# Kernel optimization log

Hardware: AMD Instinct MI355X
Metric: run time of the kernel (lower is better)

## Reference

```python
import jax, jax.numpy as jnp
import numpy as np

B, IN, OUT, N, K = 2048, 4096, 4096, 64, 4  # batch, in_features, out_features, num_nodes, degree


def setup_inputs() -> dict:
    key = jax.random.key(0)
    k0, k1, k2, k3 = jax.random.split(key, 4)
    x = jax.random.normal(k0, (B, IN), dtype=jnp.float32)
    # kaiming-ish init for the linear weight
    W = jax.random.normal(k1, (OUT, IN), dtype=jnp.float32) * (1.0 / np.sqrt(IN))
    ecoeff = jax.random.uniform(k2, (N, N), dtype=jnp.float32, minval=0.1, maxval=0.5)
    phase = jax.random.uniform(k3, (N, N), dtype=jnp.float32, minval=0.0, maxval=2.0 * np.pi)
    tension = jnp.ones((N,), dtype=jnp.float32)
    # deterministic degree-K ring topology: paths[i] = [(i+1..i+K) % N]
    src = jnp.repeat(jnp.arange(N), K).astype(jnp.int32)            # [E]
    dst = ((src + jnp.tile(jnp.arange(1, K + 1), N)) % N).astype(jnp.int32)  # [E]
    return {"x": x, "W": W, "ecoeff": ecoeff, "phase": phase,
            "tension": tension, "src": src, "dst": dst}


def reference(x, W, ecoeff, phase, tension, src, dst):
    # EntangledConnectionLayer.forward
    b = x.shape[0]
    out_features = W.shape[0]
    n = tension.shape[0]
    opn = out_features // n  # out_per_node

    out = x @ W.T  # [B, OUT] == F.linear(x, weights)
    nodes = out.reshape(b, n, opn)  # [B, N, opn] node-sliced view of output

    # entangled_connection_function on a real signal:
    # real(sig * (1 + eps*exp(i*phi)) / (1 + tau_i*tau_j)) = sig*(1+eps*cos(phi))/(1+tau_i*tau_j)
    eps = ecoeff[src, dst]                    # [E]
    phi = phase[src, dst]                     # [E]
    tau = tension[src] * tension[dst]         # [E]
    scale = (1.0 + eps * jnp.cos(phi)) / (1.0 + tau)  # [E]

    contrib = nodes[:, src, :] * scale[None, :, None]  # [B, E, opn]
    entangled = jnp.zeros_like(nodes).at[:, dst, :].add(contrib)  # scatter-add over edges

    return out + 0.5 * entangled.reshape(b, out_features)
```

## Files before the change

kernel.cpp:

```cpp
#include <hip/hip_runtime.h>
#include <hip/hip_bf16.h>

#define TILE 128
#define BK 64

typedef __attribute__((ext_vector_type(8))) short bf16x8;
typedef __attribute__((ext_vector_type(4))) float f32x4;

__device__ __forceinline__ unsigned short f32_to_bf16(float f) {
    unsigned u = __float_as_uint(f);
    unsigned rounded = u + 0x7FFF + ((u >> 16) & 1);
    return (unsigned short)(rounded >> 16);
}
__device__ __forceinline__ float bf16_to_f32(unsigned short h) {
    return __uint_as_float(((unsigned)h) << 16);
}
__device__ __forceinline__ bool probe_f32(const void* tens) {
    return ((const unsigned short*)tens)[0] == 0;
}

__global__ __launch_bounds__(256)
void prep_kernel(const void* __restrict__ xv, const void* __restrict__ Wv,
                 const void* __restrict__ ecoeff, const void* __restrict__ phase,
                 const void* __restrict__ tens,
                 const int* __restrict__ srcIdx, const int* __restrict__ dstIdx,
                 unsigned short* __restrict__ xa, unsigned short* __restrict__ wp,
                 int E, int K, int castB)
{
    constexpr int NODES = 64, CHUNK = 256, CAP = 8;
    __shared__ float buf[NODES * CHUNK];
    __shared__ int   cnt[NODES];
    __shared__ int   slist[NODES * CAP];
    __shared__ float clist[NODES * CAP];

    const bool isF32 = probe_f32(tens);
    const int tid = threadIdx.x;
    const int b   = blockIdx.x;

    if (b < castB) {
        const size_t i = ((size_t)b * 256 + tid) * 8;
        if (isF32) {
            const float4 a = *(const float4*)((const float*)xv + i);
            const float4 c = *(const float4*)((const float*)xv + i + 4);
            unsigned short p[8];
            p[0]=f32_to_bf16(a.x); p[1]=f32_to_bf16(a.y); p[2]=f32_to_bf16(a.z); p[3]=f32_to_bf16(a.w);
            p[4]=f32_to_bf16(c.x); p[5]=f32_to_bf16(c.y); p[6]=f32_to_bf16(c.z); p[7]=f32_to_bf16(c.w);
            *(bf16x8*)(xa + i) = *(const bf16x8*)p;
        } else {
            *(bf16x8*)(xa + i) = *(const bf16x8*)((const unsigned short*)xv + i);
        }
        return;
    }

    const int wb = b - castB;
    const int j  = wb & 63;
    const int k0 = (wb >> 6) * CHUNK;

    if (tid < NODES) cnt[tid] = 0;
    __syncthreads();
    if (tid < E) {
        const int s = srcIdx[tid];
        const int d = dstIdx[tid];
        float eps, phi, ts, td;
        if (isF32) {
            eps = ((const float*)ecoeff)[s * NODES + d];
            phi = ((const float*)phase)[s * NODES + d];
            ts  = ((const float*)tens)[s];
            td  = ((const float*)tens)[d];
        } else {
            eps = bf16_to_f32(((const unsigned short*)ecoeff)[s * NODES + d]);
            phi = bf16_to_f32(((const unsigned short*)phase)[s * NODES + d]);
            ts  = bf16_to_f32(((const unsigned short*)tens)[s]);
            td  = bf16_to_f32(((const unsigned short*)tens)[d]);
        }
        const float coef = 0.5f * (1.0f + eps * __cosf(phi)) / (1.0f + ts * td);
        const int pos = atomicAdd(&cnt[d], 1);
        if (pos < CAP) { slist[d * CAP + pos] = s; clist[d * CAP + pos] = coef; }
    }

    if (isF32) {
        for (int idx = tid; idx < NODES * CHUNK / 4; idx += 256) {
            const int s = idx >> 6;
            const int p = idx & 63;
            *(float4*)&buf[s * CHUNK + p * 4] = *(const float4*)
                ((const float*)Wv + (size_t)(s * 64 + j) * K + k0 + p * 4);
        }
    } else {
        for (int idx = tid; idx < NODES * CHUNK / 4; idx += 256) {
            const int s = idx >> 6;
            const int p = idx & 63;
            const ushort4 v = *(const ushort4*)
                ((const unsigned short*)Wv + (size_t)(s * 64 + j) * K + k0 + p * 4);
            buf[s * CHUNK + p * 4 + 0] = bf16_to_f32(v.x);
            buf[s * CHUNK + p * 4 + 1] = bf16_to_f32(v.y);
            buf[s * CHUNK + p * 4 + 2] = bf16_to_f32(v.z);
            buf[s * CHUNK + p * 4 + 3] = bf16_to_f32(v.w);
        }
    }
    __syncthreads();

    const int kk4  = (tid & 63) * 4;
    const int dgrp = (tid >> 6) * 16;
#pragma unroll 4
    for (int dd = 0; dd < 16; ++dd) {
        const int d = dgrp + dd;
        float v0 = buf[d * CHUNK + kk4 + 0];
        float v1 = buf[d * CHUNK + kk4 + 1];
        float v2 = buf[d * CHUNK + kk4 + 2];
        float v3 = buf[d * CHUNK + kk4 + 3];
        const int n = cnt[d] < CAP ? cnt[d] : CAP;
        for (int t = 0; t < n; ++t) {
            const float c = clist[d * CAP + t];
            const int   s = slist[d * CAP + t];
            v0 += c * buf[s * CHUNK + kk4 + 0];
            v1 += c * buf[s * CHUNK + kk4 + 1];
            v2 += c * buf[s * CHUNK + kk4 + 2];
            v3 += c * buf[s * CHUNK + kk4 + 3];
        }
        ushort4 o;
        o.x = f32_to_bf16(v0); o.y = f32_to_bf16(v1);
        o.z = f32_to_bf16(v2); o.w = f32_to_bf16(v3);
        *(ushort4*)(wp + (size_t)(d * 64 + j) * K + k0 + kk4) = o;
    }
}

__global__ __launch_bounds__(256)
void gemm_ws_kernel(const unsigned short* __restrict__ A,
                    const unsigned short* __restrict__ B,
                    void* __restrict__ Cv, const void* __restrict__ tens,
                    int M, int N, int K)
{
    __shared__ __align__(16) unsigned short As[TILE * BK];
    __shared__ __align__(16) unsigned short Bs[TILE * BK];

    const bool isF32 = probe_f32(tens);
    const int tid  = threadIdx.x;
    const int lane = tid & 63;
    const int w    = tid >> 6;
    const int wm   = (w >> 1) * 64;
    const int wn   = (w & 1) * 64;
    const int m0   = blockIdx.y * TILE;
    const int n0   = blockIdx.x * TILE;

    f32x4 acc[4][4] = {};

    const int lrow   = lane >> 3;
    const int lcolsw = ((lane & 7) ^ lrow) * 8;

    for (int k0 = 0; k0 < K; k0 += BK) {
#pragma unroll
        for (int t = 0; t < 4; ++t) {
            const int br = t * 32 + w * 8;
            const unsigned short* ga = A + (size_t)(m0 + br + lrow) * K + (k0 + lcolsw);
            const unsigned short* gb = B + (size_t)(n0 + br + lrow) * K + (k0 + lcolsw);
            __builtin_amdgcn_global_load_lds(
                (__attribute__((address_space(1))) const void*)ga,
                (__attribute__((address_space(3))) void*)&As[br * BK], 16, 0, 0);
            __builtin_amdgcn_global_load_lds(
                (__attribute__((address_space(1))) const void*)gb,
                (__attribute__((address_space(3))) void*)&Bs[br * BK], 16, 0, 0);
        }
        __syncthreads();

#pragma unroll
        for (int kk = 0; kk < BK; kk += 32) {
            const int rr = lane & 15;
            const int g  = (lane >> 4) + (kk >> 3);
            const int slot = (g ^ (rr & 7)) * 8;
            bf16x8 av[4], bv[4];
#pragma unroll
            for (int i = 0; i < 4; ++i)
                av[i] = *(const bf16x8*)&As[(wm + i * 16 + rr) * BK + slot];
#pragma unroll
            for (int i = 0; i < 4; ++i)
                bv[i] = *(const bf16x8*)&Bs[(wn + i * 16 + rr) * BK + slot];
#pragma unroll
            for (int mt = 0; mt < 4; ++mt)
#pragma unroll
                for (int nt = 0; nt < 4; ++nt)
                    acc[mt][nt] = __builtin_amdgcn_mfma_f32_16x16x32_bf16(
                        av[mt], bv[nt], acc[mt][nt], 0, 0, 0);
        }
        __syncthreads();
    }

    const int quad = (lane >> 4) * 4;
    const int col  = lane & 15;
#pragma unroll
    for (int mt = 0; mt < 4; ++mt)
#pragma unroll
        for (int nt = 0; nt < 4; ++nt)
#pragma unroll
            for (int r = 0; r < 4; ++r) {
                const size_t gr = (size_t)(m0 + wm + mt * 16 + quad + r);
                const size_t gc = (size_t)(n0 + wn + nt * 16 + col);
                const float v = acc[mt][nt][r];
                if (isF32) ((float*)Cv)[gr * N + gc] = v;
                else       ((unsigned short*)Cv)[gr * N + gc] = f32_to_bf16(v);
            }
}

__global__ __launch_bounds__(256)
void gemm_bt_kernel(const void* __restrict__ Av, const void* __restrict__ Bv,
                    void* __restrict__ Cv, const void* __restrict__ tens,
                    int M, int N, int K)
{
    __shared__ __align__(16) short As[TILE * BK];
    __shared__ __align__(16) short Bs[TILE * BK];

    const bool isF32 = probe_f32(tens);
    const int tid  = threadIdx.x;
    const int lane = tid & 63;
    const int w    = tid >> 6;
    const int wm   = (w >> 1) * 64;
    const int wn   = (w & 1) * 64;
    const int m0   = blockIdx.y * TILE;
    const int n0   = blockIdx.x * TILE;
    f32x4 acc[4][4] = {};
    const int lrow = lane >> 3;
    const int lcol = (lane & 7) * 8;

    for (int k0 = 0; k0 < K; k0 += BK) {
        if (!isF32) {
            const short* A = (const short*)Av;
            const short* B = (const short*)Bv;
#pragma unroll
            for (int t = 0; t < 4; ++t) {
                const int br = t * 32 + w * 8;
                const short* ga = A + (size_t)(m0 + br + lrow) * K + (k0 + lcol);
                const short* gb = B + (size_t)(n0 + br + lrow) * K + (k0 + lcol);
                __builtin_amdgcn_global_load_lds(
                    (__attribute__((address_space(1))) const void*)ga,
                    (__attribute__((address_space(3))) void*)&As[br * BK], 16, 0, 0);
                __builtin_amdgcn_global_load_lds(
                    (__attribute__((address_space(1))) const void*)gb,
                    (__attribute__((address_space(3))) void*)&Bs[br * BK], 16, 0, 0);
            }
        } else {
            const float* A = (const float*)Av;
            const float* B = (const float*)Bv;
#pragma unroll
            for (int t = 0; t < 4; ++t) {
                const int br = t * 32 + w * 8;
                const int row = br + lrow;
                const float* ga = A + (size_t)(m0 + row) * K + (k0 + lcol);
                const float* gb = B + (size_t)(n0 + row) * K + (k0 + lcol);
                float4 a0 = *(const float4*)(ga);
                float4 a1 = *(const float4*)(ga + 4);
                float4 b0 = *(const float4*)(gb);
                float4 b1 = *(const float4*)(gb + 4);
                short pa[8], pb[8];
                pa[0]=f32_to_bf16(a0.x); pa[1]=f32_to_bf16(a0.y);
                pa[2]=f32_to_bf16(a0.z); pa[3]=f32_to_bf16(a0.w);
                pa[4]=f32_to_bf16(a1.x); pa[5]=f32_to_bf16(a1.y);
                pa[6]=f32_to_bf16(a1.z); pa[7]=f32_to_bf16(a1.w);
                pb[0]=f32_to_bf16(b0.x); pb[1]=f32_to_bf16(b0.y);
                pb[2]=f32_to_bf16(b0.z); pb[3]=f32_to_bf16(b0.w);
                pb[4]=f32_to_bf16(b1.x); pb[5]=f32_to_bf16(b1.y);
                pb[6]=f32_to_bf16(b1.z); pb[7]=f32_to_bf16(b1.w);
                *(bf16x8*)&As[row * BK + lcol] = *(const bf16x8*)pa;
                *(bf16x8*)&Bs[row * BK + lcol] = *(const bf16x8*)pb;
            }
        }
        __syncthreads();
#pragma unroll
        for (int kk = 0; kk < BK; kk += 32) {
            const int rk = kk + (lane >> 4) * 8;
            const int rr = lane & 15;
            bf16x8 av[4], bv[4];
#pragma unroll
            for (int i = 0; i < 4; ++i)
                av[i] = *(const bf16x8*)&As[(wm + i * 16 + rr) * BK + rk];
#pragma unroll
            for (int i = 0; i < 4; ++i)
                bv[i] = *(const bf16x8*)&Bs[(wn + i * 16 + rr) * BK + rk];
#pragma unroll
            for (int mt = 0; mt < 4; ++mt)
#pragma unroll
                for (int nt = 0; nt < 4; ++nt)
                    acc[mt][nt] = __builtin_amdgcn_mfma_f32_16x16x32_bf16(
                        av[mt], bv[nt], acc[mt][nt], 0, 0, 0);
        }
        __syncthreads();
    }
    const int quad = (lane >> 4) * 4;
    const int col  = lane & 15;
#pragma unroll
    for (int mt = 0; mt < 4; ++mt)
#pragma unroll
        for (int nt = 0; nt < 4; ++nt)
#pragma unroll
            for (int r = 0; r < 4; ++r) {
                const size_t gr = (size_t)(m0 + wm + mt * 16 + quad + r);
                const size_t gc = (size_t)(n0 + wn + nt * 16 + col);
                const float v = acc[mt][nt][r];
                if (isF32) ((float*)Cv)[gr * N + gc] = v;
                else       ((unsigned short*)Cv)[gr * N + gc] = f32_to_bf16(v);
            }
}

__global__ __launch_bounds__(256)
void entangle_kernel(void* __restrict__ Cv,
                     const void* __restrict__ ecoeff,
                     const void* __restrict__ phase,
                     const void* __restrict__ tens,
                     const int* __restrict__ srcIdx,
                     const int* __restrict__ dstIdx,
                     int E)
{
    constexpr int NODES = 64, OPN = 64, FEAT = 4096, ROWS = 2, CAP = 8;
    __shared__ float rows[ROWS * FEAT];
    __shared__ int   cnt[NODES];
    __shared__ int   slist[NODES * CAP];
    __shared__ float clist[NODES * CAP];

    const bool isF32 = probe_f32(tens);
    const int tid = threadIdx.x;
    if (tid < NODES) cnt[tid] = 0;
    __syncthreads();

    if (tid < E) {
        const int s = srcIdx[tid];
        const int d = dstIdx[tid];
        float eps, phi, ts, td;
        if (isF32) {
            eps = ((const float*)ecoeff)[s * NODES + d];
            phi = ((const float*)phase)[s * NODES + d];
            ts  = ((const float*)tens)[s];
            td  = ((const float*)tens)[d];
        } else {
            eps = bf16_to_f32(((const unsigned short*)ecoeff)[s * NODES + d]);
            phi = bf16_to_f32(((const unsigned short*)phase)[s * NODES + d]);
            ts  = bf16_to_f32(((const unsigned short*)tens)[s]);
            td  = bf16_to_f32(((const unsigned short*)tens)[d]);
        }
        const float coef = 0.5f * (1.0f + eps * __cosf(phi)) / (1.0f + ts * td);
        const int pos = atomicAdd(&cnt[d], 1);
        if (pos < CAP) { slist[d * CAP + pos] = s; clist[d * CAP + pos] = coef; }
    }

    const size_t row0 = (size_t)blockIdx.x * ROWS;
    if (isF32) {
        const float4* g = (const float4*)((const float*)Cv + row0 * FEAT);
        float4* l = (float4*)rows;
        for (int i = tid; i < ROWS * FEAT / 4; i += 256) l[i] = g[i];
    } else {
        const ushort2* g = (const ushort2*)((const unsigned short*)Cv + row0 * FEAT);
        for (int i = tid; i < ROWS * FEAT / 2; i += 256) {
            const ushort2 u = g[i];
            rows[i * 2 + 0] = bf16_to_f32(u.x);
            rows[i * 2 + 1] = bf16_to_f32(u.y);
        }
    }
    __syncthreads();

    for (int c = 0; c < ROWS * FEAT / 256; ++c) {
        const int i = c * 256 + tid;
        const int r = i >> 12;
        const int o = i & (FEAT - 1);
        const int d = o >> 6;
        const int j = o & (OPN - 1);
        float v = rows[i];
        const int n = cnt[d] < CAP ? cnt[d] : CAP;
        for (int t = 0; t < n; ++t)
            v += clist[d * CAP + t] * rows[(r << 12) + slist[d * CAP + t] * OPN + j];
        if (isF32) ((float*)Cv)[(row0 + r) * FEAT + o] = v;
        else       ((unsigned short*)Cv)[(row0 + r) * FEAT + o] = f32_to_bf16(v);
    }
}

extern "C" void kernel_launch(void* const* d_in, const int* in_sizes, int n_in,
                              void* d_out, int out_size, void* d_ws, size_t ws_size,
                              hipStream_t stream)
{
    const void* x       = d_in[0];
    const void* W       = d_in[1];
    const void* ecoeff  = d_in[2];
    const void* phase   = d_in[3];
    const void* tension = d_in[4];
    const int*  src     = (const int*)d_in[5];
    const int*  dst     = (const int*)d_in[6];

    const int INF  = 4096;
    const int OUTF = 4096;
    const int M    = in_sizes[0] / INF;
    const int E    = in_sizes[5];

    const size_t needA = (size_t)M * INF * sizeof(unsigned short);
    const size_t needW = (size_t)OUTF * INF * sizeof(unsigned short);

    if (ws_size >= needA + needW) {
        unsigned short* xa = (unsigned short*)d_ws;
        unsigned short* wp = (unsigned short*)((char*)d_ws + needA);

        const int castB = (M * INF) / (256 * 8);
        const int wpB   = 64 * (INF / 256);
        prep_kernel<<<dim3(castB + wpB), dim3(256), 0, stream>>>(
            x, W, ecoeff, phase, tension, src, dst, xa, wp, E, INF, castB);
        gemm_ws_kernel<<<dim3(OUTF / TILE, M / TILE), dim3(256), 0, stream>>>(
            xa, wp, d_out, tension, M, OUTF, INF);
    } else {
        dim3 grid(OUTF / TILE, M / TILE), block(256);
        gemm_bt_kernel<<<grid, block, 0, stream>>>(x, W, d_out, tension, M, OUTF, INF);
        entangle_kernel<<<dim3(M / 2), block, 0, stream>>>(
            d_out, ecoeff, phase, tension, src, dst, E);
    }
}
```

Before: 241.9 us.

## Double GEMM K-tile to 128 and store prep weight buffer as bf16 in LDS

The GEMM main loop now stages a 128-wide K slice per iteration instead of 64. The global-to-LDS load mapping and XOR swizzle are reworked for the wider rows, which halves the number of barrier pairs per block. The prep kernel keeps its weight chunk in LDS as bf16 rather than fp32, halving that kernel's shared memory and converting values when they are read. LDS use per GEMM block doubles to 64 KB, which may cut occupancy, and fp32 weights are now rounded to bf16 before the neighbour mixing rather than after.

```diff
diff --git a/kernel.cpp b/kernel.cpp
--- a/kernel.cpp
+++ b/kernel.cpp
@@ -2,7 +2,8 @@
 #include <hip/hip_bf16.h>
 
 #define TILE 128
-#define BK 64
+#define BK   64
+#define BKG  128
 
 typedef __attribute__((ext_vector_type(8))) short bf16x8;
 typedef __attribute__((ext_vector_type(4))) float f32x4;
@@ -28,7 +29,7 @@
                  int E, int K, int castB)
 {
     constexpr int NODES = 64, CHUNK = 256, CAP = 8;
-    __shared__ float buf[NODES * CHUNK];
+    __shared__ unsigned short buf[NODES * CHUNK];
     __shared__ int   cnt[NODES];
     __shared__ int   slist[NODES * CAP];
     __shared__ float clist[NODES * CAP];
@@ -82,19 +83,19 @@
         for (int idx = tid; idx < NODES * CHUNK / 4; idx += 256) {
             const int s = idx >> 6;
             const int p = idx & 63;
-            *(float4*)&buf[s * CHUNK + p * 4] = *(const float4*)
+            const float4 v = *(const float4*)
                 ((const float*)Wv + (size_t)(s * 64 + j) * K + k0 + p * 4);
+            ushort4 u;
+            u.x = f32_to_bf16(v.x); u.y = f32_to_bf16(v.y);
+            u.z = f32_to_bf16(v.z); u.w = f32_to_bf16(v.w);
+            *(ushort4*)&buf[s * CHUNK + p * 4] = u;
         }
     } else {
         for (int idx = tid; idx < NODES * CHUNK / 4; idx += 256) {
             const int s = idx >> 6;
             const int p = idx & 63;
-            const ushort4 v = *(const ushort4*)
+            *(ushort4*)&buf[s * CHUNK + p * 4] = *(const ushort4*)
                 ((const unsigned short*)Wv + (size_t)(s * 64 + j) * K + k0 + p * 4);
-            buf[s * CHUNK + p * 4 + 0] = bf16_to_f32(v.x);
-            buf[s * CHUNK + p * 4 + 1] = bf16_to_f32(v.y);
-            buf[s * CHUNK + p * 4 + 2] = bf16_to_f32(v.z);
-            buf[s * CHUNK + p * 4 + 3] = bf16_to_f32(v.w);
         }
     }
     __syncthreads();
@@ -104,18 +105,15 @@
 #pragma unroll 4
     for (int dd = 0; dd < 16; ++dd) {
         const int d = dgrp + dd;
-        float v0 = buf[d * CHUNK + kk4 + 0];
-        float v1 = buf[d * CHUNK + kk4 + 1];
-        float v2 = buf[d * CHUNK + kk4 + 2];
-        float v3 = buf[d * CHUNK + kk4 + 3];
+        const ushort4 a = *(const ushort4*)&buf[d * CHUNK + kk4];
+        float v0 = bf16_to_f32(a.x), v1 = bf16_to_f32(a.y);
+        float v2 = bf16_to_f32(a.z), v3 = bf16_to_f32(a.w);
         const int n = cnt[d] < CAP ? cnt[d] : CAP;
         for (int t = 0; t < n; ++t) {
             const float c = clist[d * CAP + t];
-            const int   s = slist[d * CAP + t];
-            v0 += c * buf[s * CHUNK + kk4 + 0];
-            v1 += c * buf[s * CHUNK + kk4 + 1];
-            v2 += c * buf[s * CHUNK + kk4 + 2];
-            v3 += c * buf[s * CHUNK + kk4 + 3];
+            const ushort4 s4 = *(const ushort4*)&buf[slist[d * CAP + t] * CHUNK + kk4];
+            v0 += c * bf16_to_f32(s4.x); v1 += c * bf16_to_f32(s4.y);
+            v2 += c * bf16_to_f32(s4.z); v3 += c * bf16_to_f32(s4.w);
         }
         ushort4 o;
         o.x = f32_to_bf16(v0); o.y = f32_to_bf16(v1);
@@ -130,8 +128,8 @@
                     void* __restrict__ Cv, const void* __restrict__ tens,
                     int M, int N, int K)
 {
-    __shared__ __align__(16) unsigned short As[TILE * BK];
-    __shared__ __align__(16) unsigned short Bs[TILE * BK];
+    __shared__ __align__(16) unsigned short As[TILE * BKG];
+    __shared__ __align__(16) unsigned short Bs[TILE * BKG];
 
     const bool isF32 = probe_f32(tens);
     const int tid  = threadIdx.x;
@@ -144,36 +142,38 @@
 
     f32x4 acc[4][4] = {};
 
-    const int lrow   = lane >> 3;
-    const int lcolsw = ((lane & 7) ^ lrow) * 8;
-
-    for (int k0 = 0; k0 < K; k0 += BK) {
-#pragma unroll
-        for (int t = 0; t < 4; ++t) {
-            const int br = t * 32 + w * 8;
-            const unsigned short* ga = A + (size_t)(m0 + br + lrow) * K + (k0 + lcolsw);
-            const unsigned short* gb = B + (size_t)(n0 + br + lrow) * K + (k0 + lcolsw);
+    const int lrow   = lane >> 4;
+    const int lchunk = lane & 15;
+
+    for (int k0 = 0; k0 < K; k0 += BKG) {
+#pragma unroll
+        for (int t = 0; t < 8; ++t) {
+            const int br  = t * 16 + w * 4;
+            const int row = br + lrow;
+            const int gsw = ((lchunk & 7) ^ (row & 7)) | (lchunk & 8);
+            const unsigned short* ga = A + (size_t)(m0 + row) * K + (k0 + gsw * 8);
+            const unsigned short* gb = B + (size_t)(n0 + row) * K + (k0 + gsw * 8);
             __builtin_amdgcn_global_load_lds(
                 (__attribute__((address_space(1))) const void*)ga,
-                (__attribute__((address_space(3))) void*)&As[br * BK], 16, 0, 0);
+                (__attribute__((address_space(3))) void*)&As[br * BKG], 16, 0, 0);
             __builtin_amdgcn_global_load_lds(
                 (__attribute__((address_space(1))) const void*)gb,
-                (__attribute__((address_space(3))) void*)&Bs[br * BK], 16, 0, 0);
+                (__attribute__((address_space(3))) void*)&Bs[br * BKG], 16, 0, 0);
         }
         __syncthreads();
 
 #pragma unroll
-        for (int kk = 0; kk < BK; kk += 32) {
+        for (int kk = 0; kk < BKG; kk += 32) {
             const int rr = lane & 15;
-            const int g  = (lane >> 4) + (kk >> 3);
-            const int slot = (g ^ (rr & 7)) * 8;
+            const int c  = (kk >> 3) + (lane >> 4);
+            const int slot = (((c & 7) ^ (rr & 7)) | (c & 8)) * 8;
             bf16x8 av[4], bv[4];
 #pragma unroll
             for (int i = 0; i < 4; ++i)
-                av[i] = *(const bf16x8*)&As[(wm + i * 16 + rr) * BK + slot];
+                av[i] = *(const bf16x8*)&As[(wm + i * 16 + rr) * BKG + slot];
 #pragma unroll
             for (int i = 0; i < 4; ++i)
-                bv[i] = *(const bf16x8*)&Bs[(wn + i * 16 + rr) * BK + slot];
+                bv[i] = *(const bf16x8*)&Bs[(wn + i * 16 + rr) * BKG + slot];
 #pragma unroll
             for (int mt = 0; mt < 4; ++mt)
 #pragma unroll
```

New measurement: 221.4 us. -8.5%, faster.
